# Optimization experiments

Measured on AMD Instinct MI355X. Metric: run time of the kernel, lower is better.

The kernel has to match this reference:

```python
import jax, jax.numpy as jnp
import numpy as np

HEADS = 16
EMBED = 1024
HEAD_DIM = EMBED // HEADS


def setup_inputs() -> dict:
    key = jax.random.key(0)
    ks = jax.random.split(key, 10)
    B, SQ, SKV = 2, 2048, 2048
    s = 1.0 / np.sqrt(HEAD_DIM)
    sd = 1.0 / np.sqrt(EMBED)
    return {
        "queries": jax.random.normal(ks[0], (B, SQ, EMBED), jnp.float32),
        "values": jax.random.normal(ks[1], (B, SKV, EMBED), jnp.float32),
        "heads": HEADS,
        "Wv": jax.random.normal(ks[2], (HEAD_DIM, HEAD_DIM), jnp.float32) * s,
        "bv": jax.random.normal(ks[3], (HEAD_DIM,), jnp.float32) * 0.02,
        "Wk": jax.random.normal(ks[4], (HEAD_DIM, HEAD_DIM), jnp.float32) * s,
        "bk": jax.random.normal(ks[5], (HEAD_DIM,), jnp.float32) * 0.02,
        "Wq": jax.random.normal(ks[6], (HEAD_DIM, HEAD_DIM), jnp.float32) * s,
        "bq": jax.random.normal(ks[7], (HEAD_DIM,), jnp.float32) * 0.02,
        "Wd": jax.random.normal(ks[8], (EMBED, EMBED), jnp.float32) * sd,
        "bd": jax.random.normal(ks[9], (EMBED,), jnp.float32) * 0.02,
    }


def reference(queries, values, heads, Wv, bv, Wk, bk, Wq, bq, Wd, bd):
    n, sq, e = queries.shape
    skv = values.shape[1]
    d = e // heads
    # reshape to per-head layout [b, s, h, d]
    q_in = queries.reshape(n, sq, heads, d)
    v_in = values.reshape(n, skv, heads, d)
    # shared per-head linear projections (torch Linear: x @ W.T + b)
    v = jnp.einsum("bshd,ed->bshe", v_in, Wv) + bv
    # quirk preserved: keys computed from the ALREADY-PROJECTED values
    k = jnp.einsum("bshd,ed->bshe", v, Wk) + bk
    q = jnp.einsum("bshd,ed->bshe", q_in, Wq) + bq
    # full O(n^2) score matrix [b, h, sq, skv] (as in source)
    scores = jnp.einsum("bqhd,bkhd->bhqk", q, k) / jnp.sqrt(jnp.asarray(d, q.dtype))
    attn = jax.nn.softmax(scores, axis=-1)
    out = jnp.einsum("bhqk,bkhd->bqhd", attn, v).reshape(n, sq, e)
    return out @ Wd.T + bd
```

## Files before the change

### kernel.cpp

```cpp
#include <hip/hip_runtime.h>
#include <hip/hip_bf16.h>
#include <hip/hip_fp16.h>
#include <math.h>

typedef _Float16 f16;
typedef _Float16 f16x8 __attribute__((ext_vector_type(8)));
typedef _Float16 f16x4 __attribute__((ext_vector_type(4)));
typedef _Float16 f16x2 __attribute__((ext_vector_type(2)));
typedef unsigned short u16x8v __attribute__((ext_vector_type(8)));
typedef float f32x4 __attribute__((ext_vector_type(4)));

namespace {
constexpr int B = 2;
constexpr int H = 16;
constexpr int S = 2048;
constexpr int D = 64;
constexpr int E = 1024;
constexpr int LP = 72;
constexpr float QSCALE = 0.125f * 1.4426950408889634f;
}

__global__ void make_wkv(const float* __restrict__ Wk, const float* __restrict__ Wv,
                         const float* __restrict__ bv, const float* __restrict__ bk,
                         float* __restrict__ Wkv, float* __restrict__ bkv) {
  const int g = blockIdx.x * 256 + threadIdx.x;
  const int i = g >> 6, j = g & 63;
  float s = 0.f;
#pragma unroll 16
  for (int d = 0; d < 64; ++d) s = fmaf(Wk[i * 64 + d], Wv[d * 64 + j], s);
  Wkv[g] = s;
  if (g < 64) {
    float bb = bk[g];
#pragma unroll 16
    for (int d = 0; d < 64; ++d) bb = fmaf(Wk[g * 64 + d], bv[d], bb);
    bkv[g] = bb;
  }
}

__global__ __launch_bounds__(256) void cvt_wd(const float* __restrict__ W, f16* __restrict__ out) {
  const int i = blockIdx.x * 256 + threadIdx.x;
  const float4 f = ((const float4*)W)[i];
  f16x4 o;
  o.x = (f16)f.x; o.y = (f16)f.y; o.z = (f16)f.z; o.w = (f16)f.w;
  *(f16x4*)(out + 4 * (size_t)i) = o;
}

__global__ __launch_bounds__(256) void proj_mfma(const float* __restrict__ x,
                                                 const float* __restrict__ W,
                                                 const float* __restrict__ bias,
                                                 f16* __restrict__ out, float scale) {
  const int t = threadIdx.x, lane = t & 63, w = t >> 6;
  const int l15 = lane & 15, quad = lane >> 4;
  const int m0 = (blockIdx.x * 4 + w) * 64;

  f16x8 wf[4][2], af[4][2];
#pragma unroll
  for (int nt = 0; nt < 4; ++nt)
#pragma unroll
    for (int kc = 0; kc < 2; ++kc) {
      const float* g = W + (size_t)(nt * 16 + l15) * 64 + kc * 32 + quad * 8;
      const float4 a = *(const float4*)g, b2 = *(const float4*)(g + 4);
      f16x8 v;
      v[0]=(f16)a.x; v[1]=(f16)a.y; v[2]=(f16)a.z; v[3]=(f16)a.w;
      v[4]=(f16)b2.x; v[5]=(f16)b2.y; v[6]=(f16)b2.z; v[7]=(f16)b2.w;
      wf[nt][kc] = v;
    }
#pragma unroll
  for (int mt = 0; mt < 4; ++mt)
#pragma unroll
    for (int kc = 0; kc < 2; ++kc) {
      const float* g = x + (size_t)(m0 + mt * 16 + l15) * 64 + kc * 32 + quad * 8;
      const float4 a = *(const float4*)g, b2 = *(const float4*)(g + 4);
      f16x8 v;
      v[0]=(f16)a.x; v[1]=(f16)a.y; v[2]=(f16)a.z; v[3]=(f16)a.w;
      v[4]=(f16)b2.x; v[5]=(f16)b2.y; v[6]=(f16)b2.z; v[7]=(f16)b2.w;
      af[mt][kc] = v;
    }

  f32x4 acc[4][4];
#pragma unroll
  for (int mt = 0; mt < 4; ++mt)
#pragma unroll
    for (int nt = 0; nt < 4; ++nt) acc[mt][nt] = (f32x4){0.f, 0.f, 0.f, 0.f};
#pragma unroll
  for (int kc = 0; kc < 2; ++kc)
#pragma unroll
    for (int nt = 0; nt < 4; ++nt)
#pragma unroll
      for (int mt = 0; mt < 4; ++mt)
        acc[mt][nt] = __builtin_amdgcn_mfma_f32_16x16x32_f16(af[mt][kc], wf[nt][kc], acc[mt][nt], 0, 0, 0);

  float bl[4];
#pragma unroll
  for (int nt = 0; nt < 4; ++nt) bl[nt] = bias[nt * 16 + l15];

#pragma unroll
  for (int mt = 0; mt < 4; ++mt)
#pragma unroll
    for (int r = 0; r < 4; ++r) {
      const int g = m0 + mt * 16 + quad * 4 + r;
      const int h = g & 15, bs = g >> 4;
      const int b = bs >> 11, s = bs & 2047;
      f16* o = out + ((size_t)(b * H + h) * S + s) * 64;
#pragma unroll
      for (int nt = 0; nt < 4; ++nt)
        o[nt * 16 + l15] = (f16)((acc[mt][nt][r] + bl[nt]) * scale);
    }
}

__global__ __launch_bounds__(256) void attn_mfma(const f16* __restrict__ qp,
                                                 const f16* __restrict__ kp,
                                                 const f16* __restrict__ vp,
                                                 f16* __restrict__ ao) {
  __shared__ f16 ks[64 * LP];
  __shared__ f16 vt[64 * LP];
  __shared__ f16 ps[4 * 32 * LP];
  const int t = threadIdx.x, lane = t & 63, w = t >> 6;
  const int l15 = lane & 15, quad = lane >> 4;
  const int bh = blockIdx.x;
  const int q0 = blockIdx.y * 128;
  const f16* qbase = qp + ((size_t)bh * S + q0 + w * 32) * D;
  const f16* kbase = kp + (size_t)bh * S * D;
  const f16* vbase = vp + (size_t)bh * S * D;
  f16* pw = ps + w * 32 * LP;

  f16x8 qf[2][2];
#pragma unroll
  for (int mt = 0; mt < 2; ++mt)
#pragma unroll
    for (int kc = 0; kc < 2; ++kc)
      qf[mt][kc] = *(const f16x8*)(qbase + (size_t)(mt * 16 + l15) * D + kc * 32 + quad * 8);

  f16x8 vb4;
#pragma unroll
  for (int j = 0; j < 8; ++j) vb4[j] = (l15 == 0) ? (f16)1.0f : (f16)0.0f;

  f32x4 O[2][5];
#pragma unroll
  for (int mt = 0; mt < 2; ++mt)
#pragma unroll
    for (int nt = 0; nt < 5; ++nt) O[mt][nt] = (f32x4){0.f, 0.f, 0.f, 0.f};

  for (int kt = 0; kt < S / 64; ++kt) {
    __syncthreads();
    {
      const int r = t >> 2, c0 = (t & 3) * 16;
      const f16* g = kbase + ((size_t)kt * 64 + r) * D + c0;
      *(f16x8*)&ks[r * LP + c0] = *(const f16x8*)g;
      *(f16x8*)&ks[r * LP + c0 + 8] = *(const f16x8*)(g + 8);
    }
    {
      const int d0 = (t >> 5) * 8, pc0 = (t & 31) * 2;
      const int kva = (pc0 & 3) * 16 + (pc0 >> 2);
      const u16x8v a = *(const u16x8v*)(vbase + ((size_t)kt * 64 + kva) * D + d0);
      const u16x8v b2 = *(const u16x8v*)(vbase + ((size_t)kt * 64 + kva + 16) * D + d0);
#pragma unroll
      for (int j = 0; j < 8; ++j) {
        const unsigned pk = (unsigned)a[j] | ((unsigned)b2[j] << 16);
        *(unsigned*)&vt[(d0 + j) * LP + pc0] = pk;
      }
    }
    __syncthreads();

    f32x4 sc[2][4];
#pragma unroll
    for (int mt = 0; mt < 2; ++mt)
#pragma unroll
      for (int nt = 0; nt < 4; ++nt) sc[mt][nt] = (f32x4){0.f, 0.f, 0.f, 0.f};
#pragma unroll
    for (int kc = 0; kc < 2; ++kc)
#pragma unroll
      for (int nt = 0; nt < 4; ++nt) {
        const f16x8 bf = *(const f16x8*)&ks[(nt * 16 + l15) * LP + kc * 32 + quad * 8];
#pragma unroll
        for (int mt = 0; mt < 2; ++mt)
          sc[mt][nt] = __builtin_amdgcn_mfma_f32_16x16x32_f16(qf[mt][kc], bf, sc[mt][nt], 0, 0, 0);
      }

#pragma unroll
    for (int mt = 0; mt < 2; ++mt)
#pragma unroll
      for (int r = 0; r < 4; ++r) {
        const float p0 = __builtin_amdgcn_exp2f(sc[mt][0][r]);
        const float p1 = __builtin_amdgcn_exp2f(sc[mt][1][r]);
        const float p2 = __builtin_amdgcn_exp2f(sc[mt][2][r]);
        const float p3 = __builtin_amdgcn_exp2f(sc[mt][3][r]);
        union { f16x4 v4; f16x2 h[2]; } u;
        u.h[0] = __builtin_bit_cast(f16x2, __builtin_amdgcn_cvt_pkrtz(p0, p1));
        u.h[1] = __builtin_bit_cast(f16x2, __builtin_amdgcn_cvt_pkrtz(p2, p3));
        *(f16x4*)&pw[(mt * 16 + quad * 4 + r) * LP + l15 * 4] = u.v4;
      }
    __asm__ volatile("s_waitcnt lgkmcnt(0)" ::: "memory");

    f16x8 pa[2][2];
#pragma unroll
    for (int mt = 0; mt < 2; ++mt)
#pragma unroll
      for (int kc = 0; kc < 2; ++kc)
        pa[mt][kc] = *(const f16x8*)&pw[(mt * 16 + l15) * LP + kc * 32 + quad * 8];
#pragma unroll
    for (int kc = 0; kc < 2; ++kc) {
#pragma unroll
      for (int nt = 0; nt < 4; ++nt) {
        const f16x8 vbf = *(const f16x8*)&vt[(nt * 16 + l15) * LP + kc * 32 + quad * 8];
#pragma unroll
        for (int mt = 0; mt < 2; ++mt)
          O[mt][nt] = __builtin_amdgcn_mfma_f32_16x16x32_f16(pa[mt][kc], vbf, O[mt][nt], 0, 0, 0);
      }
#pragma unroll
      for (int mt = 0; mt < 2; ++mt)
        O[mt][4] = __builtin_amdgcn_mfma_f32_16x16x32_f16(pa[mt][kc], vb4, O[mt][4], 0, 0, 0);
    }
  }

  const int b = bh >> 4, h = bh & 15;
#pragma unroll
  for (int mt = 0; mt < 2; ++mt)
#pragma unroll
    for (int r = 0; r < 4; ++r) {
      const float l = __shfl(O[mt][4][r], quad << 4, 64);
      const float inv = 1.f / l;
      const int row = q0 + w * 32 + mt * 16 + quad * 4 + r;
      f16* o = ao + ((size_t)b * S + row) * E + h * D;
#pragma unroll
      for (int nt = 0; nt < 4; ++nt)
        o[nt * 16 + l15] = (f16)(O[mt][nt][r] * inv);
    }
}

__global__ __launch_bounds__(256) void dense_mfma(const f16* __restrict__ A,
                                                  const f16* __restrict__ Wd16,
                                                  const float* __restrict__ bd,
                                                  float* __restrict__ out) {
  __shared__ f16 as[128 * LP];
  __shared__ f16 bs[128 * LP];
  const int t = threadIdx.x;
  const int lane = t & 63;
  const int w = t >> 6;
  const int l15 = lane & 15;
  const int quad = lane >> 4;
  const int m0 = blockIdx.x * 128;
  const int n0 = blockIdx.y * 128;
  const int wm = (w >> 1) * 64, wn = (w & 1) * 64;

  f32x4 acc[4][4];
#pragma unroll
  for (int mt = 0; mt < 4; ++mt)
#pragma unroll
    for (int nt = 0; nt < 4; ++nt) acc[mt][nt] = (f32x4){0.f, 0.f, 0.f, 0.f};

  for (int kt = 0; kt < E / 64; ++kt) {
    __syncthreads();
    {
      const int r = t >> 1, c0 = (t & 1) * 32;
      const f16* ga = A + (size_t)(m0 + r) * E + kt * 64 + c0;
      const f16* gb = Wd16 + (size_t)(n0 + r) * E + kt * 64 + c0;
#pragma unroll
      for (int c = 0; c < 4; ++c) {
        *(f16x8*)&as[r * LP + c0 + 8 * c] = *(const f16x8*)(ga + 8 * c);
        *(f16x8*)&bs[r * LP + c0 + 8 * c] = *(const f16x8*)(gb + 8 * c);
      }
    }
    __syncthreads();
    f16x8 af[4][2];
#pragma unroll
    for (int mt = 0; mt < 4; ++mt)
#pragma unroll
      for (int kc = 0; kc < 2; ++kc)
        af[mt][kc] = *(const f16x8*)&as[(wm + mt * 16 + l15) * LP + kc * 32 + quad * 8];
#pragma unroll
    for (int kc = 0; kc < 2; ++kc)
#pragma unroll
      for (int nt = 0; nt < 4; ++nt) {
        const f16x8 bf = *(const f16x8*)&bs[(wn + nt * 16 + l15) * LP + kc * 32 + quad * 8];
#pragma unroll
        for (int mt = 0; mt < 4; ++mt)
          acc[mt][nt] = __builtin_amdgcn_mfma_f32_16x16x32_f16(af[mt][kc], bf, acc[mt][nt], 0, 0, 0);
      }
  }
#pragma unroll
  for (int nt = 0; nt < 4; ++nt) {
    const int col = n0 + wn + nt * 16 + l15;
    const float bdv = bd[col];
#pragma unroll
    for (int mt = 0; mt < 4; ++mt)
#pragma unroll
      for (int r = 0; r < 4; ++r)
        out[(size_t)(m0 + wm + mt * 16 + quad * 4 + r) * E + col] = acc[mt][nt][r] + bdv;
  }
}

extern "C" void kernel_launch(void* const* d_in, const int* in_sizes, int n_in,
                              void* d_out, int out_size, void* d_ws, size_t ws_size,
                              hipStream_t stream) {
  const float* queries = (const float*)d_in[0];
  const float* values  = (const float*)d_in[1];
  const float* Wv = (const float*)d_in[3];
  const float* bv = (const float*)d_in[4];
  const float* Wk = (const float*)d_in[5];
  const float* bk = (const float*)d_in[6];
  const float* Wq = (const float*)d_in[7];
  const float* bq = (const float*)d_in[8];
  const float* Wd = (const float*)d_in[9];
  const float* bd = (const float*)d_in[10];
  float* out = (float*)d_out;

  char* ws = (char*)d_ws;
  f16* qp    = (f16*)(ws);
  f16* kp    = (f16*)(ws + 8u * 1024 * 1024);
  f16* vp    = (f16*)(ws + 16u * 1024 * 1024);
  f16* ao    = (f16*)(ws + 24u * 1024 * 1024);
  f16* wd16  = (f16*)(ws + 32u * 1024 * 1024);
  float* wkv = (float*)(ws + 34u * 1024 * 1024);
  float* bkv = (float*)(ws + 34u * 1024 * 1024 + 16384);
  (void)ws_size; (void)in_sizes; (void)n_in; (void)out_size;

  make_wkv<<<16, 256, 0, stream>>>(Wk, Wv, bv, bk, wkv, bkv);
  cvt_wd<<<E * E / 1024, 256, 0, stream>>>(Wd, wd16);
  proj_mfma<<<256, 256, 0, stream>>>(queries, Wq, bq, qp, QSCALE);
  proj_mfma<<<256, 256, 0, stream>>>(values, Wv, bv, vp, 1.0f);
  proj_mfma<<<256, 256, 0, stream>>>(values, wkv, bkv, kp, 1.0f);
  attn_mfma<<<dim3(B * H, S / 128), 256, 0, stream>>>(qp, kp, vp, ao);
  dense_mfma<<<dim3(B * S / 128, E / 128), 256, 0, stream>>>(ao, wd16, bd, out);
}
```

Before: 198.6 us.

## Split attention over KV halves, fuse V/K projections, convert Wd inline

Attention now runs with a split over the key/value range (grid z = 2), writing unnormalized fp32 partial outputs and row sums, which a new combine kernel adds and normalizes into the fp16 attention output. This doubles the number of attention blocks to raise occupancy on the GPU, at the cost of extra fp32 partial traffic and one more launch. Because softmax uses no running max, adding the partial sums is exact. The V and K projections are fused into one kernel that reads the values input once, and the separate Wd conversion kernel is removed in favour of converting fp32 weights while loading tiles in the dense GEMM. The output buffer is reused as scratch for the second partial.

```diff
diff --git a/kernel.cpp b/kernel.cpp
--- a/kernel.cpp
+++ b/kernel.cpp
@@ -17,6 +17,7 @@
 constexpr int D = 64;
 constexpr int E = 1024;
 constexpr int LP = 72;
+constexpr int NSPLIT = 2;
 constexpr float QSCALE = 0.125f * 1.4426950408889634f;
 }
 
@@ -37,14 +38,6 @@
   }
 }
 
-__global__ __launch_bounds__(256) void cvt_wd(const float* __restrict__ W, f16* __restrict__ out) {
-  const int i = blockIdx.x * 256 + threadIdx.x;
-  const float4 f = ((const float4*)W)[i];
-  f16x4 o;
-  o.x = (f16)f.x; o.y = (f16)f.y; o.z = (f16)f.z; o.w = (f16)f.w;
-  *(f16x4*)(out + 4 * (size_t)i) = o;
-}
-
 __global__ __launch_bounds__(256) void proj_mfma(const float* __restrict__ x,
                                                  const float* __restrict__ W,
                                                  const float* __restrict__ bias,
@@ -108,10 +101,95 @@
     }
 }
 
+__global__ __launch_bounds__(256) void proj_vk_mfma(const float* __restrict__ x,
+                                                    const float* __restrict__ Wv,
+                                                    const float* __restrict__ bv,
+                                                    const float* __restrict__ Wkv,
+                                                    const float* __restrict__ bkv,
+                                                    f16* __restrict__ vout,
+                                                    f16* __restrict__ kout) {
+  const int t = threadIdx.x, lane = t & 63, w = t >> 6;
+  const int l15 = lane & 15, quad = lane >> 4;
+  const int m0 = (blockIdx.x * 4 + w) * 32;
+
+  f16x8 wfv[4][2], wfk[4][2], af[2][2];
+#pragma unroll
+  for (int nt = 0; nt < 4; ++nt)
+#pragma unroll
+    for (int kc = 0; kc < 2; ++kc) {
+      const size_t off = (size_t)(nt * 16 + l15) * 64 + kc * 32 + quad * 8;
+      {
+        const float4 a = *(const float4*)(Wv + off), b2 = *(const float4*)(Wv + off + 4);
+        f16x8 v;
+        v[0]=(f16)a.x; v[1]=(f16)a.y; v[2]=(f16)a.z; v[3]=(f16)a.w;
+        v[4]=(f16)b2.x; v[5]=(f16)b2.y; v[6]=(f16)b2.z; v[7]=(f16)b2.w;
+        wfv[nt][kc] = v;
+      }
+      {
+        const float4 a = *(const float4*)(Wkv + off), b2 = *(const float4*)(Wkv + off + 4);
+        f16x8 v;
+        v[0]=(f16)a.x; v[1]=(f16)a.y; v[2]=(f16)a.z; v[3]=(f16)a.w;
+        v[4]=(f16)b2.x; v[5]=(f16)b2.y; v[6]=(f16)b2.z; v[7]=(f16)b2.w;
+        wfk[nt][kc] = v;
+      }
+    }
+#pragma unroll
+  for (int mt = 0; mt < 2; ++mt)
+#pragma unroll
+    for (int kc = 0; kc < 2; ++kc) {
+      const float* g = x + (size_t)(m0 + mt * 16 + l15) * 64 + kc * 32 + quad * 8;
+      const float4 a = *(const float4*)g, b2 = *(const float4*)(g + 4);
+      f16x8 v;
+      v[0]=(f16)a.x; v[1]=(f16)a.y; v[2]=(f16)a.z; v[3]=(f16)a.w;
+      v[4]=(f16)b2.x; v[5]=(f16)b2.y; v[6]=(f16)b2.z; v[7]=(f16)b2.w;
+      af[mt][kc] = v;
+    }
+
+  f32x4 accv[2][4], acck[2][4];
+#pragma unroll
+  for (int mt = 0; mt < 2; ++mt)
+#pragma unroll
+    for (int nt = 0; nt < 4; ++nt) {
+      accv[mt][nt] = (f32x4){0.f, 0.f, 0.f, 0.f};
+      acck[mt][nt] = (f32x4){0.f, 0.f, 0.f, 0.f};
+    }
+#pragma unroll
+  for (int kc = 0; kc < 2; ++kc)
+#pragma unroll
+    for (int nt = 0; nt < 4; ++nt)
+#pragma unroll
+      for (int mt = 0; mt < 2; ++mt) {
+        accv[mt][nt] = __builtin_amdgcn_mfma_f32_16x16x32_f16(af[mt][kc], wfv[nt][kc], accv[mt][nt], 0, 0, 0);
+        acck[mt][nt] = __builtin_amdgcn_mfma_f32_16x16x32_f16(af[mt][kc], wfk[nt][kc], acck[mt][nt], 0, 0, 0);
+      }
+
+  float blv[4], blk[4];
+#pragma unroll
+  for (int nt = 0; nt < 4; ++nt) { blv[nt] = bv[nt * 16 + l15]; blk[nt] = bkv[nt * 16 + l15]; }
+
+#pragma unroll
+  for (int mt = 0; mt < 2; ++mt)
+#pragma unroll
+    for (int r = 0; r < 4; ++r) {
+      const int g = m0 + mt * 16 + quad * 4 + r;
+      const int h = g & 15, bs = g >> 4;
+      const int b = bs >> 11, s = bs & 2047;
+      const size_t o = ((size_t)(b * H + h) * S + s) * 64;
+#pragma unroll
+      for (int nt = 0; nt < 4; ++nt) {
+        vout[o + nt * 16 + l15] = (f16)(accv[mt][nt][r] + blv[nt]);
+        kout[o + nt * 16 + l15] = (f16)(acck[mt][nt][r] + blk[nt]);
+      }
+    }
+}
+
 __global__ __launch_bounds__(256) void attn_mfma(const f16* __restrict__ qp,
                                                  const f16* __restrict__ kp,
                                                  const f16* __restrict__ vp,
-                                                 f16* __restrict__ ao) {
+                                                 float* __restrict__ part0,
+                                                 float* __restrict__ part1,
+                                                 float* __restrict__ lp0,
+                                                 float* __restrict__ lp1) {
   __shared__ f16 ks[64 * LP];
   __shared__ f16 vt[64 * LP];
   __shared__ f16 ps[4 * 32 * LP];
@@ -119,6 +197,7 @@
   const int l15 = lane & 15, quad = lane >> 4;
   const int bh = blockIdx.x;
   const int q0 = blockIdx.y * 128;
+  const int split = blockIdx.z;
   const f16* qbase = qp + ((size_t)bh * S + q0 + w * 32) * D;
   const f16* kbase = kp + (size_t)bh * S * D;
   const f16* vbase = vp + (size_t)bh * S * D;
@@ -141,7 +220,9 @@
 #pragma unroll
     for (int nt = 0; nt < 5; ++nt) O[mt][nt] = (f32x4){0.f, 0.f, 0.f, 0.f};
 
-  for (int kt = 0; kt < S / 64; ++kt) {
+  const int kt0 = split * (S / 64 / NSPLIT);
+  const int kt1 = kt0 + (S / 64 / NSPLIT);
+  for (int kt = kt0; kt < kt1; ++kt) {
     __syncthreads();
     {
       const int r = t >> 2, c0 = (t & 3) * 16;
@@ -198,6 +279,7 @@
 #pragma unroll
       for (int kc = 0; kc < 2; ++kc)
         pa[mt][kc] = *(const f16x8*)&pw[(mt * 16 + l15) * LP + kc * 32 + quad * 8];
+
 #pragma unroll
     for (int kc = 0; kc < 2; ++kc) {
 #pragma unroll
@@ -213,23 +295,46 @@
     }
   }
 
-  const int b = bh >> 4, h = bh & 15;
+  float* Opart = split ? part1 : part0;
+  float* Lpart = split ? lp1 : lp0;
 #pragma unroll
   for (int mt = 0; mt < 2; ++mt)
 #pragma unroll
     for (int r = 0; r < 4; ++r) {
       const float l = __shfl(O[mt][4][r], quad << 4, 64);
-      const float inv = 1.f / l;
       const int row = q0 + w * 32 + mt * 16 + quad * 4 + r;
-      f16* o = ao + ((size_t)b * S + row) * E + h * D;
+      float* o = Opart + ((size_t)bh * S + row) * 64;
 #pragma unroll
       for (int nt = 0; nt < 4; ++nt)
-        o[nt * 16 + l15] = (f16)(O[mt][nt][r] * inv);
-    }
+        o[nt * 16 + l15] = O[mt][nt][r];
+      if (l15 == 0) Lpart[(size_t)bh * S + row] = l;
+    }
+}
+
+__global__ __launch_bounds__(256) void combine_attn(const float* __restrict__ p0,
+                                                    const float* __restrict__ p1,
+                                                    const float* __restrict__ l0,
+                                                    const float* __restrict__ l1,
+                                                    f16* __restrict__ ao) {
+  const int i = blockIdx.x * 256 + threadIdx.x;
+  const size_t e0 = (size_t)i * 4;
+  const int row = (int)(e0 >> 6);
+  const int d = (int)(e0 & 63);
+  const float inv = 1.f / (l0[row] + l1[row]);
+  const float4 a = *(const float4*)(p0 + e0);
+  const float4 b2 = *(const float4*)(p1 + e0);
+  const int bh = row >> 11, q = row & 2047;
+  const int b = bh >> 4, h = bh & 15;
+  f16x4 o;
+  o.x = (f16)((a.x + b2.x) * inv);
+  o.y = (f16)((a.y + b2.y) * inv);
+  o.z = (f16)((a.z + b2.z) * inv);
+  o.w = (f16)((a.w + b2.w) * inv);
+  *(f16x4*)(ao + ((size_t)b * S + q) * E + h * 64 + d) = o;
 }
 
 __global__ __launch_bounds__(256) void dense_mfma(const f16* __restrict__ A,
-                                                  const f16* __restrict__ Wd16,
+                                                  const float* __restrict__ Wd,
                                                   const float* __restrict__ bd,
                                                   float* __restrict__ out) {
   __shared__ f16 as[128 * LP];
@@ -254,11 +359,17 @@
     {
       const int r = t >> 1, c0 = (t & 1) * 32;
       const f16* ga = A + (size_t)(m0 + r) * E + kt * 64 + c0;
-      const f16* gb = Wd16 + (size_t)(n0 + r) * E + kt * 64 + c0;
+      const float* gb = Wd + (size_t)(n0 + r) * E + kt * 64 + c0;
+#pragma unroll
+      for (int c = 0; c < 4; ++c)
+        *(f16x8*)&as[r * LP + c0 + 8 * c] = *(const f16x8*)(ga + 8 * c);
 #pragma unroll
       for (int c = 0; c < 4; ++c) {
-        *(f16x8*)&as[r * LP + c0 + 8 * c] = *(const f16x8*)(ga + 8 * c);
-        *(f16x8*)&bs[r * LP + c0 + 8 * c] = *(const f16x8*)(gb + 8 * c);
+        const float4 a = *(const float4*)(gb + 8 * c), b2 = *(const float4*)(gb + 8 * c + 4);
+        f16x8 v;
+        v[0]=(f16)a.x; v[1]=(f16)a.y; v[2]=(f16)a.z; v[3]=(f16)a.w;
+        v[4]=(f16)b2.x; v[5]=(f16)b2.y; v[6]=(f16)b2.z; v[7]=(f16)b2.w;
+        *(f16x8*)&bs[r * LP + c0 + 8 * c] = v;
       }
     }
     __syncthreads();
@@ -310,16 +421,18 @@
   f16* kp    = (f16*)(ws + 8u * 1024 * 1024);
   f16* vp    = (f16*)(ws + 16u * 1024 * 1024);
   f16* ao    = (f16*)(ws + 24u * 1024 * 1024);
-  f16* wd16  = (f16*)(ws + 32u * 1024 * 1024);
-  float* wkv = (float*)(ws + 34u * 1024 * 1024);
-  float* bkv = (float*)(ws + 34u * 1024 * 1024 + 16384);
+  float* wkv = (float*)(ws + 32u * 1024 * 1024);
+  float* bkv = (float*)(ws + 32u * 1024 * 1024 + 16384);
+  float* lp0 = (float*)(ws + 33u * 1024 * 1024);
+  float* lp1 = (float*)(ws + 33u * 1024 * 1024 + 256 * 1024);
+  float* p0  = (float*)(ws + 34u * 1024 * 1024);
+  float* p1  = out;
   (void)ws_size; (void)in_sizes; (void)n_in; (void)out_size;
 
   make_wkv<<<16, 256, 0, stream>>>(Wk, Wv, bv, bk, wkv, bkv);
-  cvt_wd<<<E * E / 1024, 256, 0, stream>>>(Wd, wd16);
   proj_mfma<<<256, 256, 0, stream>>>(queries, Wq, bq, qp, QSCALE);
-  proj_mfma<<<256, 256, 0, stream>>>(values, Wv, bv, vp, 1.0f);
-  proj_mfma<<<256, 256, 0, stream>>>(values, wkv, bkv, kp, 1.0f);
-  attn_mfma<<<dim3(B * H, S / 128), 256, 0, stream>>>(qp, kp, vp, ao);
-  dense_mfma<<<dim3(B * S / 128, E / 128), 256, 0, stream>>>(ao, wd16, bd, out);
-}
+  proj_vk_mfma<<<512, 256, 0, stream>>>(values, Wv, bv, wkv, bkv, vp, kp);
+  attn_mfma<<<dim3(B * H, S / 128, NSPLIT), 256, 0, stream>>>(qp, kp, vp, p0, p1, lp0, lp1);
+  combine_attn<<<B * H * S * D / (4 * 256), 256, 0, stream>>>(p0, p1, lp0, lp1, ao);
+  dense_mfma<<<dim3(B * S / 128, E / 128), 256, 0, stream>>>(ao, Wd, bd, out);
+}
```

Result: slower. 219.4 us (+10.5%).
